# Optimization experiments

Measured on AMD Instinct MI355X. Metric: run time of the kernel, lower is better.

The kernel has to match this reference:

```python
import jax, jax.numpy as jnp
import numpy as np

BLOCK = 32          # MX block size along the contraction dim
E4M3_MAX = 448.0    # max finite magnitude of float8_e4m3fn
E4M3_MAX_EXP = 8.0  # floor(log2(448)) = 8


def mxfp8_quant_dequant(t):
    """Simulate MXFP8 (OCP MX spec): per-32-block E8M0 power-of-two scale,
    elements cast to float8_e4m3fn, then dequantized back to fp32."""
    orig_shape = t.shape
    tb = t.reshape(-1, BLOCK)
    amax = jnp.max(jnp.abs(tb), axis=-1, keepdims=True)
    # E8M0 shared scale: 2^(floor(log2(amax)) - emax_e4m3)
    exp = jnp.floor(jnp.log2(jnp.maximum(amax, 2.0 ** -126))) - E4M3_MAX_EXP
    scale = jnp.exp2(exp)
    q = jnp.clip(tb / scale, -E4M3_MAX, E4M3_MAX)
    q = q.astype(jnp.float8_e4m3fn).astype(t.dtype)  # round-to-nearest fp8
    return (q * scale).reshape(orig_shape)


def setup_inputs() -> dict:
    key = jax.random.key(0)
    k1, k2, k3 = jax.random.split(key, 3)
    B, S, D_IN, D_OUT = 4, 4096, 4096, 4096
    x = jax.random.normal(k1, (B, S, D_IN), dtype=jnp.float32)
    weight = jax.random.normal(k2, (D_OUT, D_IN), dtype=jnp.float32) * 0.02
    bias = jax.random.normal(k3, (D_OUT,), dtype=jnp.float32) * 0.02
    return {"x": x, "weight": weight, "bias": bias}


def reference(x, weight, bias):
    B, S, D_IN = x.shape
    # Inline activation quantization to MXFP8 (blocks of 32 along in_features)
    x2 = x.reshape(-1, D_IN)                 # [B*S, D_IN]
    x_dq = mxfp8_quant_dequant(x2)
    # Weight is stored MXFP8-quantized; dequantize with its block scales
    w_dq = mxfp8_quant_dequant(weight)       # [D_OUT, D_IN]
    out = jnp.einsum('nk,ok->no', x_dq, w_dq) + bias  # microscaled GEMM
    return out.reshape(B, S, -1)
```

## Files before the change

### kernel.cpp

```cpp
#include <hip/hip_runtime.h>
#include <hip/hip_bf16.h>
#include <stdint.h>

typedef __attribute__((ext_vector_type(8))) short bf16x8;
typedef __attribute__((ext_vector_type(4))) float f32x4;
typedef __attribute__((ext_vector_type(8))) unsigned short u16x8;

#define BM 256
#define BN 256
#define BKT 32
#define ABYTES (BM * BKT * 2)
#define BBYTES (BN * BKT * 2)
#define BUFBYTES (ABYTES + BBYTES)
#define NBUF 4

__device__ __forceinline__ float mx_qd_elem(float x, int e) {
    float xs = ldexpf(x, -e);
    xs = fminf(448.f, fmaxf(-448.f, xs));
    float a = fabsf(xs);
    float r;
    if (a < 0.015625f) {
        r = ldexpf(rintf(ldexpf(a, 9)), -9);
    } else {
        int E = (int)((__float_as_uint(a) >> 23) & 0xFF) - 127;
        r = ldexpf(rintf(ldexpf(a, 3 - E)), E - 3);
    }
    r = copysignf(r, xs);
    return ldexpf(r, e);
}

__global__ __launch_bounds__(256) void mx_quant_bf16(
    const float* __restrict__ in, uint16_t* __restrict__ out, int nblk) {
    int t = blockIdx.x * 256 + threadIdx.x;
    if (t >= nblk) return;
    const float4* p = (const float4*)(in + (size_t)t * 32);
    float v[32];
#pragma unroll
    for (int i = 0; i < 8; ++i) {
        float4 fv = p[i];
        v[4 * i + 0] = fv.x; v[4 * i + 1] = fv.y;
        v[4 * i + 2] = fv.z; v[4 * i + 3] = fv.w;
    }
    float amax = 0.f;
#pragma unroll
    for (int i = 0; i < 32; ++i) amax = fmaxf(amax, fabsf(v[i]));
    amax = fmaxf(amax, 1.17549435e-38f);
    int e = (int)((__float_as_uint(amax) >> 23) & 0xFF) - 127 - 8;

    unsigned short res[32];
#pragma unroll
    for (int i = 0; i < 32; ++i) {
        float d = mx_qd_elem(v[i], e);
        res[i] = (unsigned short)(__float_as_uint(d) >> 16);
    }
    u16x8* o = (u16x8*)(out + (size_t)t * 32);
#pragma unroll
    for (int j = 0; j < 4; ++j) {
        u16x8 pack;
#pragma unroll
        for (int i = 0; i < 8; ++i) pack[i] = res[8 * j + i];
        o[j] = pack;
    }
}

#define GLOAD(srcp, ldsoff)                                                     \
    __builtin_amdgcn_global_load_lds(                                           \
        (const __attribute__((address_space(1))) void*)(srcp),                  \
        (__attribute__((address_space(3))) void*)&lds[ldsoff], 16, 0, 0)

__global__ __launch_bounds__(512, 2) void gemm_d2_bf16(
    const uint16_t* __restrict__ A, const uint16_t* __restrict__ B,
    const float* __restrict__ bias, float* __restrict__ C,
    int Nrows, int K, int O) {
    __shared__ __align__(16) uint8_t lds[NBUF * BUFBYTES];

    const int tid  = threadIdx.x;
    const int lane = tid & 63;
    const int w    = tid >> 6;
    const int f    = lane & 15, g = lane >> 4;
    const int wm   = w >> 2,    wn = w & 3;

    const int nwg  = gridDim.x * gridDim.y;
    const int flat = blockIdx.y * gridDim.x + blockIdx.x;
    const int swz  = (flat & 7) * (nwg >> 3) + (flat >> 3);
    const int bx   = swz % gridDim.x, by = swz / gridDim.x;
    const int rowBase = by * BM, colBase = bx * BN;

    const int srow = tid >> 2;
    const int ssc  = ((tid & 3) ^ ((srow >> 1) & 3)) * 16;
    const size_t K2 = (size_t)K * 2;
    const uint8_t* gA0 = (const uint8_t*)A + (size_t)(rowBase + srow) * K2 + ssc;
    const uint8_t* gA1 = (const uint8_t*)A + (size_t)(rowBase + 128 + srow) * K2 + ssc;
    const uint8_t* gB0 = (const uint8_t*)B + (size_t)(colBase + srow) * K2 + ssc;
    const uint8_t* gB1 = (const uint8_t*)B + (size_t)(colBase + 128 + srow) * K2 + ssc;
    const int sld = tid * 16;
#define STAGE(t) do {                                                           \
        const int _buf = ((t) & 3) * BUFBYTES;                                  \
        const size_t _kb = (size_t)(t) * (BKT * 2);                             \
        GLOAD(gA0 + _kb, _buf + sld);                                           \
        GLOAD(gA1 + _kb, _buf + 8192 + sld);                                    \
        GLOAD(gB0 + _kb, _buf + ABYTES + sld);                                  \
        GLOAD(gB1 + _kb, _buf + ABYTES + 8192 + sld);                           \
    } while (0)

    int aoff[8], boff[4];
#pragma unroll
    for (int m = 0; m < 8; ++m) {
        int r = wm * 128 + m * 16 + f;
        aoff[m] = r * 64 + ((g ^ ((r >> 1) & 3)) * 16);
    }
#pragma unroll
    for (int n = 0; n < 4; ++n) {
        int r = wn * 64 + n * 16 + f;
        boff[n] = ABYTES + r * 64 + ((g ^ ((r >> 1) & 3)) * 16);
    }

    f32x4 acc[8][4];
#pragma unroll
    for (int m = 0; m < 8; ++m)
#pragma unroll
        for (int n = 0; n < 4; ++n)
#pragma unroll
            for (int j = 0; j < 4; ++j) acc[m][n][j] = 0.f;

    const int nt = K / BKT;

#define WAITL(N) do {                                                           \
        asm volatile("s_waitcnt lgkmcnt(" #N ")" ::: "memory");                 \
        __builtin_amdgcn_sched_barrier(0);                                      \
    } while (0)
#define MFMA_C(MB, AF, BF) do {                                                 \
        __builtin_amdgcn_s_setprio(1);                                          \
        _Pragma("unroll") for (int _m = 0; _m < 4; ++_m)                        \
        _Pragma("unroll") for (int _n = 0; _n < 4; ++_n)                        \
            acc[(MB) + _m][_n] = __builtin_amdgcn_mfma_f32_16x16x32_bf16(       \
                AF[_m], BF[_n], acc[(MB) + _m][_n], 0, 0, 0);                   \
        __builtin_amdgcn_s_setprio(0);                                          \
    } while (0)

    STAGE(0);
    STAGE(1);
    asm volatile("s_waitcnt vmcnt(4)" ::: "memory");
    __builtin_amdgcn_sched_barrier(0);
    __builtin_amdgcn_s_barrier();
    __builtin_amdgcn_sched_barrier(0);

    for (int t = 0; t < nt; ++t) {
        const int bb = (t & 3) * BUFBYTES;
        const bool pf = (t + 2) < nt;
        bf16x8 bA[4], aLo[4], aHi[4];

#pragma unroll
        for (int n = 0; n < 4; ++n) bA[n] = *(const bf16x8*)&lds[bb + boff[n]];
#pragma unroll
        for (int m = 0; m < 4; ++m) aLo[m] = *(const bf16x8*)&lds[bb + aoff[m]];
#pragma unroll
        for (int m = 0; m < 4; ++m) aHi[m] = *(const bf16x8*)&lds[bb + aoff[4 + m]];
        if (pf) STAGE(t + 2);
        WAITL(4);
        MFMA_C(0, aLo, bA);
        WAITL(0);
        MFMA_C(4, aHi, bA);
        if (pf) asm volatile("s_waitcnt vmcnt(4)" ::: "memory");
        else    asm volatile("s_waitcnt vmcnt(0)" ::: "memory");
        __builtin_amdgcn_sched_barrier(0);
        __builtin_amdgcn_s_barrier();
        __builtin_amdgcn_sched_barrier(0);
    }
#undef STAGE
#undef WAITL
#undef MFMA_C

    const int qr = g * 4;
#pragma unroll
    for (int n = 0; n < 4; ++n) {
        int col = colBase + wn * 64 + n * 16 + f;
        float bv = bias[col];
#pragma unroll
        for (int m = 0; m < 8; ++m) {
            int r0 = rowBase + wm * 128 + m * 16 + qr;
#pragma unroll
            for (int j = 0; j < 4; ++j)
                C[(size_t)(r0 + j) * O + col] = acc[m][n][j] + bv;
        }
    }
}

extern "C" void kernel_launch(void* const* d_in, const int* in_sizes, int n_in,
                              void* d_out, int out_size, void* d_ws, size_t ws_size,
                              hipStream_t stream) {
    const float* x    = (const float*)d_in[0];
    const float* wgt  = (const float*)d_in[1];
    const float* bias = (const float*)d_in[2];
    float* out = (float*)d_out;

    const int D_OUT = in_sizes[2];
    const int D_IN  = in_sizes[1] / D_OUT;
    const int NROWS = in_sizes[0] / D_IN;

    uint16_t* xq = (uint16_t*)d_ws;
    uint16_t* wq = xq + (size_t)NROWS * D_IN;

    int nblkx = NROWS * (D_IN / 32);
    int nblkw = D_OUT * (D_IN / 32);
    mx_quant_bf16<<<dim3((nblkx + 255) / 256), dim3(256), 0, stream>>>(x, xq, nblkx);
    mx_quant_bf16<<<dim3((nblkw + 255) / 256), dim3(256), 0, stream>>>(wgt, wq, nblkw);

    dim3 grid(D_OUT / BN, NROWS / BM);
    gemm_d2_bf16<<<grid, dim3(512), 0, stream>>>(xq, wq, bias, out,
                                                 NROWS, D_IN, D_OUT);
}
```

Before: 630.5 us.

## Deepen global prefetch to three stages and software-pipeline LDS fragment loads

```diff
diff --git a/kernel.cpp b/kernel.cpp
--- a/kernel.cpp
+++ b/kernel.cpp
@@ -68,7 +68,7 @@
         (const __attribute__((address_space(1))) void*)(srcp),                  \
         (__attribute__((address_space(3))) void*)&lds[ldsoff], 16, 0, 0)
 
-__global__ __launch_bounds__(512, 2) void gemm_d2_bf16(
+__global__ __launch_bounds__(512, 2) void gemm_p3_bf16(
     const uint16_t* __restrict__ A, const uint16_t* __restrict__ B,
     const float* __restrict__ bias, float* __restrict__ C,
     int Nrows, int K, int O) {
@@ -138,38 +138,49 @@
         __builtin_amdgcn_s_setprio(0);                                          \
     } while (0)
 
-    STAGE(0);
-    STAGE(1);
+    bf16x8 bA0[4], aLo0[4], bA1[4], aLo1[4], aHi[4];
+
+#define TILE_BODY(t, bAc, aLoc, bAn, aLon) do {                                 \
+        const int bb = ((t) & 3) * BUFBYTES;                                    \
+        _Pragma("unroll") for (int _m = 0; _m < 4; ++_m)                        \
+            aHi[_m] = *(const bf16x8*)&lds[bb + aoff[4 + _m]];                  \
+        WAITL(4);                                                               \
+        if ((t) + 1 < nt) {                                                     \
+            const int bb1 = (((t) + 1) & 3) * BUFBYTES;                         \
+            _Pragma("unroll") for (int _n = 0; _n < 4; ++_n)                    \
+                bAn[_n] = *(const bf16x8*)&lds[bb1 + boff[_n]];                 \
+            _Pragma("unroll") for (int _m = 0; _m < 4; ++_m)                    \
+                aLon[_m] = *(const bf16x8*)&lds[bb1 + aoff[_m]];                \
+        }                                                                       \
+        MFMA_C(0, aLoc, bAc);                                                   \
+        if ((t) + 1 < nt) WAITL(8); else WAITL(0);                              \
+        if ((t) + 3 < nt) STAGE((t) + 3);                                       \
+        MFMA_C(4, aHi, bAc);                                                    \
+        if ((t) + 3 < nt) asm volatile("s_waitcnt vmcnt(4)" ::: "memory");      \
+        else              asm volatile("s_waitcnt vmcnt(0)" ::: "memory");      \
+        __builtin_amdgcn_sched_barrier(0);                                      \
+        __builtin_amdgcn_s_barrier();                                           \
+        __builtin_amdgcn_sched_barrier(0);                                      \
+    } while (0)
+
+    STAGE(0); STAGE(1); STAGE(2);
     asm volatile("s_waitcnt vmcnt(4)" ::: "memory");
     __builtin_amdgcn_sched_barrier(0);
     __builtin_amdgcn_s_barrier();
     __builtin_amdgcn_sched_barrier(0);
-
-    for (int t = 0; t < nt; ++t) {
-        const int bb = (t & 3) * BUFBYTES;
-        const bool pf = (t + 2) < nt;
-        bf16x8 bA[4], aLo[4], aHi[4];
-
-#pragma unroll
-        for (int n = 0; n < 4; ++n) bA[n] = *(const bf16x8*)&lds[bb + boff[n]];
-#pragma unroll
-        for (int m = 0; m < 4; ++m) aLo[m] = *(const bf16x8*)&lds[bb + aoff[m]];
-#pragma unroll
-        for (int m = 0; m < 4; ++m) aHi[m] = *(const bf16x8*)&lds[bb + aoff[4 + m]];
-        if (pf) STAGE(t + 2);
-        WAITL(4);
-        MFMA_C(0, aLo, bA);
-        WAITL(0);
-        MFMA_C(4, aHi, bA);
-        if (pf) asm volatile("s_waitcnt vmcnt(4)" ::: "memory");
-        else    asm volatile("s_waitcnt vmcnt(0)" ::: "memory");
-        __builtin_amdgcn_sched_barrier(0);
-        __builtin_amdgcn_s_barrier();
-        __builtin_amdgcn_sched_barrier(0);
+#pragma unroll
+    for (int n = 0; n < 4; ++n) bA0[n] = *(const bf16x8*)&lds[boff[n]];
+#pragma unroll
+    for (int m = 0; m < 4; ++m) aLo0[m] = *(const bf16x8*)&lds[aoff[m]];
+
+    for (int tt = 0; tt < nt; tt += 2) {
+        TILE_BODY(tt,     bA0, aLo0, bA1, aLo1);
+        TILE_BODY(tt + 1, bA1, aLo1, bA0, aLo0);
     }
 #undef STAGE
 #undef WAITL
 #undef MFMA_C
+#undef TILE_BODY
 
     const int qr = g * 4;
 #pragma unroll
@@ -207,6 +218,6 @@
     mx_quant_bf16<<<dim3((nblkw + 255) / 256), dim3(256), 0, stream>>>(wgt, wq, nblkw);
 
     dim3 grid(D_OUT / BN, NROWS / BM);
-    gemm_d2_bf16<<<grid, dim3(512), 0, stream>>>(xq, wq, bias, out,
+    gemm_p3_bf16<<<grid, dim3(512), 0, stream>>>(xq, wq, bias, out,
                                                  NROWS, D_IN, D_OUT);
 }
```

After: 636.3 us. Within noise of the previous version (+0.9%).
